# Kernel tuning notes

Hardware: AMD Instinct MI355X
Metric: run time of the kernel (lower is better)

Reference implementation:

```python
import jax, jax.numpy as jnp
import numpy as np

N_NODES = 20000
N_EDGES = 320000
IN_CH = 512
HEADS = 4
OUT_CH = 128
NEG_SLOPE = 0.2  # PyG GATConv default leaky_relu slope


def setup_inputs() -> dict:
    key = jax.random.key(0)
    k1, k2, k3, k4, k5 = jax.random.split(key, 5)
    x = jax.random.normal(k1, (N_NODES, IN_CH), dtype=jnp.float32)
    edge_index = jax.random.randint(k2, (2, N_EDGES), 0, N_NODES, dtype=jnp.int64)
    # Learned parameters (glorot-ish scaling)
    W = jax.random.normal(k3, (IN_CH, HEADS * OUT_CH), dtype=jnp.float32) * np.float32(1.0 / np.sqrt(IN_CH))
    att_src = jax.random.normal(k4, (HEADS, OUT_CH), dtype=jnp.float32) * np.float32(0.1)
    att_dst = jax.random.normal(k5, (HEADS, OUT_CH), dtype=jnp.float32) * np.float32(0.1)
    bias = jnp.zeros((OUT_CH,), dtype=jnp.float32)
    return {"x": x, "W": W, "att_src": att_src, "att_dst": att_dst, "bias": bias, "edge_index": edge_index}


def reference(x, W, att_src, att_dst, bias, edge_index):
    N = x.shape[0]
    H, C = att_src.shape
    # add self-loops (PyG GATConv default add_self_loops=True)
    loop = jnp.arange(N, dtype=edge_index.dtype)
    ei = jnp.concatenate([edge_index, jnp.stack([loop, loop])], axis=1)
    src, dst = ei[0], ei[1]
    # linear projection: [N, H, C]
    xl = (x @ W).reshape(N, H, C)
    # per-node attention halves: [N, H]
    a_s = jnp.einsum('nhc,hc->nh', xl, att_src)
    a_d = jnp.einsum('nhc,hc->nh', xl, att_dst)
    # per-edge logits + segment softmax over incoming edges (grouped by dst)
    alpha = jax.nn.leaky_relu(a_s[src] + a_d[dst], negative_slope=NEG_SLOPE)  # [E, H]
    amax = jax.ops.segment_max(alpha, dst, num_segments=N)  # every node has a self-loop -> no empty segments
    ae = jnp.exp(alpha - amax[dst])
    denom = jax.ops.segment_sum(ae, dst, num_segments=N)
    alpha = ae / (denom[dst] + 1e-16)
    # weighted scatter-add of source features: [N, H, C]
    out = jax.ops.segment_sum(alpha[:, :, None] * xl[src], dst, num_segments=N)
    # concat=False -> mean over heads, then bias [C]
    out = out.mean(axis=1) + bias
    return jax.nn.elu(out)
```

## Files before the change

### kernel.cpp

```cpp
#include <hip/hip_runtime.h>
#include <math.h>

#define N_NODES 20000
#define N_PAD 20096
#define N_EDGES 320000
#define IN_CH 512
#define HEADS 4
#define OUT_CH 128
#define HC 512
#define NEG_SLOPE 0.2f

#define CVX_BLOCKS 5024
#define CVW_BLOCKS 64
#define CNT_BLOCKS 1250
#define ATT_BLOCKS 1250

typedef __attribute__((ext_vector_type(8))) short short8;
typedef __attribute__((ext_vector_type(4))) float float4v;

__device__ __forceinline__ int detect_is64(const int* __restrict__ ei32) {
    int is64 = 1;
    #pragma unroll
    for (int i = 0; i < 32; i++) is64 &= (ei32[2 * i + 1] == 0);
    return is64;
}

__device__ __forceinline__ int edge_at(const void* ei, int is64, long long idx) {
    return is64 ? (int)((const long long*)ei)[idx] : ((const int*)ei)[idx];
}

__device__ __forceinline__ unsigned short f2bf(float f) {
    union { float f; unsigned u; } v; v.f = f;
    unsigned r = v.u + 0x7fffu + ((v.u >> 16) & 1u);
    return (unsigned short)(r >> 16);
}

__device__ __forceinline__ void bf8_decode(uint4 r, float* f) {
    f[0] = __uint_as_float(r.x << 16); f[1] = __uint_as_float(r.x & 0xffff0000u);
    f[2] = __uint_as_float(r.y << 16); f[3] = __uint_as_float(r.y & 0xffff0000u);
    f[4] = __uint_as_float(r.z << 16); f[5] = __uint_as_float(r.z & 0xffff0000u);
    f[6] = __uint_as_float(r.w << 16); f[7] = __uint_as_float(r.w & 0xffff0000u);
}

__device__ __forceinline__ float leaky(float t) { return t > 0.f ? t : NEG_SLOPE * t; }

__device__ __forceinline__ float sel_head(float4 w, int hd) {
    float lo = (hd & 1) ? w.y : w.x;
    float hi = (hd & 1) ? w.w : w.z;
    return (hd & 2) ? hi : lo;
}

__global__ __launch_bounds__(256) void fusedA_kernel(const float* __restrict__ x,
                                                     const float* __restrict__ W,
                                                     unsigned short* __restrict__ xb,
                                                     unsigned short* __restrict__ Wt,
                                                     const void* __restrict__ ei,
                                                     int* __restrict__ counts) {
    __shared__ float tile[64][65];
    int b = blockIdx.x;
    if (b < CVX_BLOCKS) {
        size_t i = ((size_t)b * 256 + threadIdx.x) * 8;
        unsigned short o[8];
        if (i < (size_t)N_NODES * IN_CH) {
            float4 f0 = *(const float4*)&x[i];
            float4 f1 = *(const float4*)&x[i + 4];
            o[0] = f2bf(f0.x); o[1] = f2bf(f0.y); o[2] = f2bf(f0.z); o[3] = f2bf(f0.w);
            o[4] = f2bf(f1.x); o[5] = f2bf(f1.y); o[6] = f2bf(f1.z); o[7] = f2bf(f1.w);
        } else {
            for (int k = 0; k < 8; k++) o[k] = 0;
        }
        *(short8*)&xb[i] = *(short8*)o;
    } else if (b < CVX_BLOCKS + CVW_BLOCKS) {
        int idx = b - CVX_BLOCKS;
        int k0 = (idx & 7) * 64, n0 = (idx >> 3) * 64;
        int t = threadIdx.x, r = t >> 6, c = t & 63;
        for (int rr = r; rr < 64; rr += 4)
            tile[rr][c] = W[(size_t)(k0 + rr) * HC + n0 + c];
        __syncthreads();
        for (int rr = r; rr < 64; rr += 4)
            Wt[(size_t)(n0 + rr) * IN_CH + k0 + c] = f2bf(tile[c][rr]);
    } else {
        int is64 = detect_is64((const int*)ei);
        int e = (b - CVX_BLOCKS - CVW_BLOCKS) * 256 + threadIdx.x;
        if (e < N_EDGES) {
            int dst = edge_at(ei, is64, (long long)N_EDGES + e);
            atomicAdd(&counts[dst], 1);
        }
    }
}

__global__ __launch_bounds__(256) void gemm_kernel(const unsigned short* __restrict__ A,
                                                   const unsigned short* __restrict__ Bt,
                                                   unsigned short* __restrict__ Cb) {
    __shared__ __align__(16) unsigned short As[128 * 32];
    __shared__ __align__(16) unsigned short Bs[128 * 32];
    const int bm = blockIdx.y * 128;
    const int bn = blockIdx.x * 128;
    const int t = threadIdx.x;
    const int wv = t >> 6, lane = t & 63;
    const int wm = wv & 1, wn = wv >> 1;
    const int lm = lane & 15, lk = lane >> 4;

    float4v acc[4][4];
    #pragma unroll
    for (int i = 0; i < 4; i++)
        #pragma unroll
        for (int j = 0; j < 4; j++) acc[i][j] = (float4v){0.f, 0.f, 0.f, 0.f};

    const int srow = t >> 2;
    const int skof = (t & 3) * 8;

    for (int k0 = 0; k0 < IN_CH; k0 += 32) {
        __syncthreads();
        #pragma unroll
        for (int q = 0; q < 2; q++) {
            const unsigned short* gA = A + (size_t)(bm + q * 64 + srow) * IN_CH + k0 + skof;
            const unsigned short* gB = Bt + (size_t)(bn + q * 64 + srow) * IN_CH + k0 + skof;
            __builtin_amdgcn_global_load_lds((const __attribute__((address_space(1))) void*)gA,
                                             (__attribute__((address_space(3))) void*)&As[q * 2048 + t * 8], 16, 0, 0);
            __builtin_amdgcn_global_load_lds((const __attribute__((address_space(1))) void*)gB,
                                             (__attribute__((address_space(3))) void*)&Bs[q * 2048 + t * 8], 16, 0, 0);
        }
        __syncthreads();

        short8 af[4], bf[4];
        #pragma unroll
        for (int i = 0; i < 4; i++)
            af[i] = *(const short8*)&As[(wm * 64 + i * 16 + lm) * 32 + lk * 8];
        #pragma unroll
        for (int j = 0; j < 4; j++)
            bf[j] = *(const short8*)&Bs[(wn * 64 + j * 16 + lm) * 32 + lk * 8];
        #pragma unroll
        for (int i = 0; i < 4; i++)
            #pragma unroll
            for (int j = 0; j < 4; j++)
                acc[i][j] = __builtin_amdgcn_mfma_f32_16x16x32_bf16(af[i], bf[j], acc[i][j], 0, 0, 0);
    }

    #pragma unroll
    for (int i = 0; i < 4; i++) {
        #pragma unroll
        for (int r = 0; r < 4; r++) {
            int row = bm + wm * 64 + i * 16 + lk * 4 + r;
            if (row < N_NODES) {
                #pragma unroll
                for (int j = 0; j < 4; j++) {
                    int col = bn + wn * 64 + j * 16 + lm;
                    Cb[(size_t)row * HC + col] = f2bf(acc[i][j][r]);
                }
            }
        }
    }
}

__global__ __launch_bounds__(1024) void scanattn_kernel(const int* __restrict__ counts,
                                                        int* __restrict__ offsets,
                                                        const unsigned short* __restrict__ xlb,
                                                        const float* __restrict__ att_s,
                                                        const float* __restrict__ att_d,
                                                        float* __restrict__ a_s,
                                                        float* __restrict__ a_d) {
    int b = blockIdx.x;
    if (b == 0) {
        const int CHUNK = 20;
        int tid = threadIdx.x;
        int base = tid * CHUNK;
        int c[CHUNK];
        #pragma unroll
        for (int k = 0; k < CHUNK; k++) {
            int i = base + k;
            c[k] = (i < N_NODES) ? counts[i] : 0;
        }
        int pre[CHUNK];
        int sum = 0;
        #pragma unroll
        for (int k = 0; k < CHUNK; k++) { pre[k] = sum; sum += c[k]; }

        int lane = tid & 63, wvv = tid >> 6;
        int s = sum;
        #pragma unroll
        for (int off = 1; off < 64; off <<= 1) {
            int u = __shfl_up(s, off, 64);
            if (lane >= off) s += u;
        }
        __shared__ int wsum[16];
        if (lane == 63) wsum[wvv] = s;
        __syncthreads();
        if (tid < 16) {
            int u = wsum[tid];
            #pragma unroll
            for (int off = 1; off < 16; off <<= 1) {
                int w = __shfl_up(u, off, 64);
                if (tid >= off) u += w;
            }
            wsum[tid] = u;
        }
        __syncthreads();
        int wbase = (wvv == 0) ? 0 : wsum[wvv - 1];
        int excl = wbase + s - sum;
        #pragma unroll
        for (int k = 0; k < CHUNK; k++) {
            int i = base + k;
            if (i < N_NODES) offsets[i] = excl + pre[k];
        }
        if (tid == 1023) offsets[N_NODES] = wbase + s;
    } else {
        int node = (b - 1) * 16 + (threadIdx.x >> 6);
        if (node >= N_NODES) return;
        int lane = threadIdx.x & 63;
        int hd = lane >> 4;
        uint4 r = *(const uint4*)&xlb[(size_t)node * HC + lane * 8];
        float f[8];
        bf8_decode(r, f);
        float4 s0 = *(const float4*)&att_s[lane * 8];
        float4 s1 = *(const float4*)&att_s[lane * 8 + 4];
        float4 d0 = *(const float4*)&att_d[lane * 8];
        float4 d1 = *(const float4*)&att_d[lane * 8 + 4];
        float s = f[0]*s0.x + f[1]*s0.y + f[2]*s0.z + f[3]*s0.w
                + f[4]*s1.x + f[5]*s1.y + f[6]*s1.z + f[7]*s1.w;
        float d = f[0]*d0.x + f[1]*d0.y + f[2]*d0.z + f[3]*d0.w
                + f[4]*d1.x + f[5]*d1.y + f[6]*d1.z + f[7]*d1.w;
        #pragma unroll
        for (int off = 1; off < 16; off <<= 1) {
            s += __shfl_xor(s, off, 64);
            d += __shfl_xor(d, off, 64);
        }
        if ((lane & 15) == 0) {
            a_s[node * 4 + hd] = s;
            a_d[node * 4 + hd] = d;
        }
    }
}

__global__ __launch_bounds__(256) void scatterw_kernel(const void* __restrict__ ei,
                                                       const int* __restrict__ offsets,
                                                       int* __restrict__ cursor,
                                                       int* __restrict__ sorted_src,
                                                       const float* __restrict__ a_s,
                                                       const float* __restrict__ a_d,
                                                       float* __restrict__ edge_w) {
    int is64 = detect_is64((const int*)ei);
    int e = blockIdx.x * 256 + threadIdx.x;
    if (e < N_EDGES) {
        int dst = edge_at(ei, is64, (long long)N_EDGES + e);
        int src = edge_at(ei, is64, e);
        int pos = offsets[dst] + atomicAdd(&cursor[dst], 1);
        sorted_src[pos] = src;
        float4 as4 = *(const float4*)&a_s[src * 4];
        float4 ad4 = *(const float4*)&a_d[dst * 4];
        float4 w;
        w.x = __expf(leaky(as4.x + ad4.x));
        w.y = __expf(leaky(as4.y + ad4.y));
        w.z = __expf(leaky(as4.z + ad4.z));
        w.w = __expf(leaky(as4.w + ad4.w));
        *(float4*)&edge_w[(size_t)pos * 4] = w;
    }
}

__global__ __launch_bounds__(256) void gather_kernel(const unsigned short* __restrict__ xlb,
                                                     const float* __restrict__ a_s,
                                                     const float* __restrict__ a_d,
                                                     const int* __restrict__ offsets,
                                                     const int* __restrict__ sorted_src,
                                                     const float* __restrict__ edge_w,
                                                     const float* __restrict__ bias,
                                                     float* __restrict__ out) {
    __shared__ float cl[2][64][9];
    int wv = threadIdx.x >> 6;
    int nib = wv >> 1;
    int sub = wv & 1;
    int node = blockIdx.x * 2 + nib;
    int lane = threadIdx.x & 63;
    int hd = lane >> 4;
    int beg = offsets[node], end = offsets[node + 1];

    const unsigned short* xrow = xlb + lane * 8;
    float acc[8] = {0, 0, 0, 0, 0, 0, 0, 0};
    float denom = 0.f;

    if (sub == 0) {
        float4 as4 = *(const float4*)&a_s[node * 4];
        float4 ad4 = *(const float4*)&a_d[node * 4];
        float4 ws;
        ws.x = __expf(leaky(as4.x + ad4.x));
        ws.y = __expf(leaky(as4.y + ad4.y));
        ws.z = __expf(leaky(as4.z + ad4.z));
        ws.w = __expf(leaky(as4.w + ad4.w));
        float w = sel_head(ws, hd);
        denom = w;
        uint4 r = *(const uint4*)(xrow + (size_t)node * HC);
        float f[8];
        bf8_decode(r, f);
        #pragma unroll
        for (int k = 0; k < 8; k++) acc[k] = w * f[k];
    }

    for (int c0 = beg + sub * 4; c0 < end; c0 += 8) {
        int n = end - c0;
        if (n >= 4) {
            int s0 = sorted_src[c0];
            int s1 = sorted_src[c0 + 1];
            int s2 = sorted_src[c0 + 2];
            int s3 = sorted_src[c0 + 3];
            uint4 r0 = *(const uint4*)(xrow + (size_t)s0 * HC);
            uint4 r1 = *(const uint4*)(xrow + (size_t)s1 * HC);
            uint4 r2 = *(const uint4*)(xrow + (size_t)s2 * HC);
            uint4 r3 = *(const uint4*)(xrow + (size_t)s3 * HC);
            float4 wa = *(const float4*)&edge_w[(size_t)c0 * 4];
            float4 wb = *(const float4*)&edge_w[(size_t)(c0 + 1) * 4];
            float4 wc = *(const float4*)&edge_w[(size_t)(c0 + 2) * 4];
            float4 wd = *(const float4*)&edge_w[(size_t)(c0 + 3) * 4];
            float w0 = sel_head(wa, hd), w1 = sel_head(wb, hd);
            float w2 = sel_head(wc, hd), w3 = sel_head(wd, hd);
            denom += (w0 + w1) + (w2 + w3);
            float f0[8], f1[8], f2[8], f3[8];
            bf8_decode(r0, f0);
            bf8_decode(r1, f1);
            bf8_decode(r2, f2);
            bf8_decode(r3, f3);
            #pragma unroll
            for (int k = 0; k < 8; k++)
                acc[k] += (w0 * f0[k] + w1 * f1[k]) + (w2 * f2[k] + w3 * f3[k]);
        } else {
            for (int j = 0; j < n; j++) {
                int s0 = sorted_src[c0 + j];
                uint4 r0 = *(const uint4*)(xrow + (size_t)s0 * HC);
                float4 wa = *(const float4*)&edge_w[(size_t)(c0 + j) * 4];
                float w0 = sel_head(wa, hd);
                denom += w0;
                float f0[8];
                bf8_decode(r0, f0);
                #pragma unroll
                for (int k = 0; k < 8; k++) acc[k] += w0 * f0[k];
            }
        }
    }

    if (sub == 1) {
        #pragma unroll
        for (int k = 0; k < 8; k++) cl[nib][lane][k] = acc[k];
        cl[nib][lane][8] = denom;
    }
    __syncthreads();
    if (sub == 0) {
        #pragma unroll
        for (int k = 0; k < 8; k++) acc[k] += cl[nib][lane][k];
        denom += cl[nib][lane][8];

        float rd = 0.25f / (denom + 1e-16f);
        float v[8];
        #pragma unroll
        for (int k = 0; k < 8; k++) {
            float t = acc[k] * rd;
            t += __shfl_xor(t, 16, 64);
            t += __shfl_xor(t, 32, 64);
            v[k] = t;
        }
        if (hd == 0) {
            float4 b0 = *(const float4*)&bias[lane * 8];
            float4 b1 = *(const float4*)&bias[lane * 8 + 4];
            float o[8];
            o[0] = v[0] + b0.x; o[1] = v[1] + b0.y; o[2] = v[2] + b0.z; o[3] = v[3] + b0.w;
            o[4] = v[4] + b1.x; o[5] = v[5] + b1.y; o[6] = v[6] + b1.z; o[7] = v[7] + b1.w;
            #pragma unroll
            for (int k = 0; k < 8; k++) o[k] = o[k] > 0.f ? o[k] : expm1f(o[k]);
            *(float4*)&out[(size_t)node * OUT_CH + lane * 8]     = make_float4(o[0], o[1], o[2], o[3]);
            *(float4*)&out[(size_t)node * OUT_CH + lane * 8 + 4] = make_float4(o[4], o[5], o[6], o[7]);
        }
    }
}

extern "C" void kernel_launch(void* const* d_in, const int* in_sizes, int n_in,
                              void* d_out, int out_size, void* d_ws, size_t ws_size,
                              hipStream_t stream) {
    const float* x       = (const float*)d_in[0];
    const float* W       = (const float*)d_in[1];
    const float* att_src = (const float*)d_in[2];
    const float* att_dst = (const float*)d_in[3];
    const float* bias    = (const float*)d_in[4];
    const void*  ei      = d_in[5];
    float* out = (float*)d_out;

    char* ws = (char*)d_ws;
    size_t off = 0;
    unsigned short* xlb = (unsigned short*)(ws + off); off += (size_t)N_PAD * HC * sizeof(unsigned short);
    float* a_s     = (float*)(ws + off); off += (size_t)N_NODES * HEADS * sizeof(float);
    float* a_d     = (float*)(ws + off); off += (size_t)N_NODES * HEADS * sizeof(float);
    int* counts    = (int*)(ws + off);   off += (size_t)N_NODES * sizeof(int);
    int* cursor    = (int*)(ws + off);   off += (size_t)N_NODES * sizeof(int);
    int* offsets   = (int*)(ws + off);   off += (size_t)(N_NODES + 1) * sizeof(int);
    off = (off + 15) & ~(size_t)15;
    int* sorted_src = (int*)(ws + off);  off += (size_t)N_EDGES * sizeof(int);
    off = (off + 15) & ~(size_t)15;
    float* edge_w  = (float*)(ws + off); off += (size_t)N_EDGES * HEADS * sizeof(float);
    unsigned short* xb = (unsigned short*)(ws + off); off += (size_t)N_PAD * IN_CH * sizeof(unsigned short);
    unsigned short* Wt = (unsigned short*)(ws + off); off += (size_t)IN_CH * HC * sizeof(unsigned short);

    hipMemsetAsync(counts, 0, 2u * N_NODES * sizeof(int), stream);
    fusedA_kernel<<<CVX_BLOCKS + CVW_BLOCKS + CNT_BLOCKS, 256, 0, stream>>>(x, W, xb, Wt, ei, counts);
    gemm_kernel<<<dim3(HC / 128, N_PAD / 128), 256, 0, stream>>>(xb, Wt, xlb);
    scanattn_kernel<<<1 + ATT_BLOCKS, 1024, 0, stream>>>(counts, offsets, xlb, att_src, att_dst, a_s, a_d);
    scatterw_kernel<<<(N_EDGES + 255) / 256, 256, 0, stream>>>(ei, offsets, cursor, sorted_src, a_s, a_d, edge_w);
    gather_kernel<<<N_NODES / 2, 256, 0, stream>>>(xlb, a_s, a_d, offsets, sorted_src, edge_w, bias, out);
}
```

Baseline: 215.3 us.

## Fuse x bf16 conversion and attention dot-products into GEMM with full-width tiles

The GEMM now reads fp32 x directly and converts it to bf16 while staging into LDS, which removes the separate conversion pass and the xb intermediate buffer. Each block covers 64 rows across all 512 output columns, so the per-head attention dot products a_s and a_d are computed from the accumulators in the epilogue. This eliminates the attention pass that re-read xlb. The cost is that the A-tile staging uses a synchronous register path instead of direct global-to-LDS loads. The scan moves to its own single-block kernel, and the attention scores are computed from fp32 accumulators instead of the rounded bf16 output.

```diff
diff --git a/kernel.cpp b/kernel.cpp
--- a/kernel.cpp
+++ b/kernel.cpp
@@ -2,7 +2,7 @@
 #include <math.h>
 
 #define N_NODES 20000
-#define N_PAD 20096
+#define N_PAD64 20032
 #define N_EDGES 320000
 #define IN_CH 512
 #define HEADS 4
@@ -10,10 +10,12 @@
 #define HC 512
 #define NEG_SLOPE 0.2f
 
-#define CVX_BLOCKS 5024
+#define GEMM_BM 64
+#define GEMM_BK 32
+#define GRID_M 313
+
 #define CVW_BLOCKS 64
 #define CNT_BLOCKS 1250
-#define ATT_BLOCKS 1250
 
 typedef __attribute__((ext_vector_type(8))) short short8;
 typedef __attribute__((ext_vector_type(4))) float float4v;
@@ -50,29 +52,14 @@
     return (hd & 2) ? hi : lo;
 }
 
-__global__ __launch_bounds__(256) void fusedA_kernel(const float* __restrict__ x,
-                                                     const float* __restrict__ W,
-                                                     unsigned short* __restrict__ xb,
+__global__ __launch_bounds__(256) void fusedA_kernel(const float* __restrict__ W,
                                                      unsigned short* __restrict__ Wt,
                                                      const void* __restrict__ ei,
                                                      int* __restrict__ counts) {
     __shared__ float tile[64][65];
     int b = blockIdx.x;
-    if (b < CVX_BLOCKS) {
-        size_t i = ((size_t)b * 256 + threadIdx.x) * 8;
-        unsigned short o[8];
-        if (i < (size_t)N_NODES * IN_CH) {
-            float4 f0 = *(const float4*)&x[i];
-            float4 f1 = *(const float4*)&x[i + 4];
-            o[0] = f2bf(f0.x); o[1] = f2bf(f0.y); o[2] = f2bf(f0.z); o[3] = f2bf(f0.w);
-            o[4] = f2bf(f1.x); o[5] = f2bf(f1.y); o[6] = f2bf(f1.z); o[7] = f2bf(f1.w);
-        } else {
-            for (int k = 0; k < 8; k++) o[k] = 0;
-        }
-        *(short8*)&xb[i] = *(short8*)o;
-    } else if (b < CVX_BLOCKS + CVW_BLOCKS) {
-        int idx = b - CVX_BLOCKS;
-        int k0 = (idx & 7) * 64, n0 = (idx >> 3) * 64;
+    if (b < CVW_BLOCKS) {
+        int k0 = (b & 7) * 64, n0 = (b >> 3) * 64;
         int t = threadIdx.x, r = t >> 6, c = t & 63;
         for (int rr = r; rr < 64; rr += 4)
             tile[rr][c] = W[(size_t)(k0 + rr) * HC + n0 + c];
@@ -81,7 +68,7 @@
             Wt[(size_t)(n0 + rr) * IN_CH + k0 + c] = f2bf(tile[c][rr]);
     } else {
         int is64 = detect_is64((const int*)ei);
-        int e = (b - CVX_BLOCKS - CVW_BLOCKS) * 256 + threadIdx.x;
+        int e = (b - CVW_BLOCKS) * 256 + threadIdx.x;
         if (e < N_EDGES) {
             int dst = edge_at(ei, is64, (long long)N_EDGES + e);
             atomicAdd(&counts[dst], 1);
@@ -89,16 +76,20 @@
     }
 }
 
-__global__ __launch_bounds__(256) void gemm_kernel(const unsigned short* __restrict__ A,
-                                                   const unsigned short* __restrict__ Bt,
-                                                   unsigned short* __restrict__ Cb) {
-    __shared__ __align__(16) unsigned short As[128 * 32];
-    __shared__ __align__(16) unsigned short Bs[128 * 32];
-    const int bm = blockIdx.y * 128;
-    const int bn = blockIdx.x * 128;
+__global__ __launch_bounds__(512) void gemm_kernel(const float* __restrict__ x,
+                                                   const unsigned short* __restrict__ Wt,
+                                                   unsigned short* __restrict__ Cb,
+                                                   const float* __restrict__ att_s_g,
+                                                   const float* __restrict__ att_d_g,
+                                                   float* __restrict__ a_s,
+                                                   float* __restrict__ a_d) {
+    __shared__ __align__(16) unsigned short As[GEMM_BM * GEMM_BK];
+    __shared__ __align__(16) unsigned short Bs[HC * GEMM_BK];
+    __shared__ float red_s[8][GEMM_BM];
+    __shared__ float red_d[8][GEMM_BM];
+    const int bm = blockIdx.x * GEMM_BM;
     const int t = threadIdx.x;
     const int wv = t >> 6, lane = t & 63;
-    const int wm = wv & 1, wn = wv >> 1;
     const int lm = lane & 15, lk = lane >> 4;
 
     float4v acc[4][4];
@@ -107,29 +98,35 @@
         #pragma unroll
         for (int j = 0; j < 4; j++) acc[i][j] = (float4v){0.f, 0.f, 0.f, 0.f};
 
-    const int srow = t >> 2;
-    const int skof = (t & 3) * 8;
-
-    for (int k0 = 0; k0 < IN_CH; k0 += 32) {
+    const int arow = t >> 3;
+    const int akof = (t & 7) * 4;
+    const int agrow = bm + arow;
+
+    for (int k0 = 0; k0 < IN_CH; k0 += GEMM_BK) {
         __syncthreads();
-        #pragma unroll
-        for (int q = 0; q < 2; q++) {
-            const unsigned short* gA = A + (size_t)(bm + q * 64 + srow) * IN_CH + k0 + skof;
-            const unsigned short* gB = Bt + (size_t)(bn + q * 64 + srow) * IN_CH + k0 + skof;
-            __builtin_amdgcn_global_load_lds((const __attribute__((address_space(1))) void*)gA,
-                                             (__attribute__((address_space(3))) void*)&As[q * 2048 + t * 8], 16, 0, 0);
+        float4 av = make_float4(0.f, 0.f, 0.f, 0.f);
+        if (agrow < N_NODES) av = *(const float4*)&x[(size_t)agrow * IN_CH + k0 + akof];
+        uint2 ap;
+        ap.x = (unsigned)f2bf(av.x) | ((unsigned)f2bf(av.y) << 16);
+        ap.y = (unsigned)f2bf(av.z) | ((unsigned)f2bf(av.w) << 16);
+        *(uint2*)&As[arow * GEMM_BK + akof] = ap;
+        #pragma unroll
+        for (int q = 0; q < 4; q++) {
+            int c = q * 512 + t;
+            int n = c >> 2, k8 = (c & 3) * 8;
+            const unsigned short* gB = Wt + (size_t)n * IN_CH + k0 + k8;
             __builtin_amdgcn_global_load_lds((const __attribute__((address_space(1))) void*)gB,
-                                             (__attribute__((address_space(3))) void*)&Bs[q * 2048 + t * 8], 16, 0, 0);
+                                             (__attribute__((address_space(3))) void*)&Bs[n * GEMM_BK + k8], 16, 0, 0);
         }
         __syncthreads();
 
         short8 af[4], bf[4];
         #pragma unroll
         for (int i = 0; i < 4; i++)
-            af[i] = *(const short8*)&As[(wm * 64 + i * 16 + lm) * 32 + lk * 8];
+            af[i] = *(const short8*)&As[(i * 16 + lm) * GEMM_BK + lk * 8];
         #pragma unroll
         for (int j = 0; j < 4; j++)
-            bf[j] = *(const short8*)&Bs[(wn * 64 + j * 16 + lm) * 32 + lk * 8];
+            bf[j] = *(const short8*)&Bs[(wv * 64 + j * 16 + lm) * GEMM_BK + lk * 8];
         #pragma unroll
         for (int i = 0; i < 4; i++)
             #pragma unroll
@@ -141,95 +138,98 @@
     for (int i = 0; i < 4; i++) {
         #pragma unroll
         for (int r = 0; r < 4; r++) {
-            int row = bm + wm * 64 + i * 16 + lk * 4 + r;
+            int row = bm + i * 16 + lk * 4 + r;
             if (row < N_NODES) {
                 #pragma unroll
                 for (int j = 0; j < 4; j++) {
-                    int col = bn + wn * 64 + j * 16 + lm;
+                    int col = wv * 64 + j * 16 + lm;
                     Cb[(size_t)row * HC + col] = f2bf(acc[i][j][r]);
                 }
             }
         }
     }
-}
-
-__global__ __launch_bounds__(1024) void scanattn_kernel(const int* __restrict__ counts,
-                                                        int* __restrict__ offsets,
-                                                        const unsigned short* __restrict__ xlb,
-                                                        const float* __restrict__ att_s,
-                                                        const float* __restrict__ att_d,
-                                                        float* __restrict__ a_s,
-                                                        float* __restrict__ a_d) {
-    int b = blockIdx.x;
-    if (b == 0) {
-        const int CHUNK = 20;
-        int tid = threadIdx.x;
-        int base = tid * CHUNK;
-        int c[CHUNK];
-        #pragma unroll
-        for (int k = 0; k < CHUNK; k++) {
-            int i = base + k;
-            c[k] = (i < N_NODES) ? counts[i] : 0;
-        }
-        int pre[CHUNK];
-        int sum = 0;
-        #pragma unroll
-        for (int k = 0; k < CHUNK; k++) { pre[k] = sum; sum += c[k]; }
-
-        int lane = tid & 63, wvv = tid >> 6;
-        int s = sum;
-        #pragma unroll
-        for (int off = 1; off < 64; off <<= 1) {
-            int u = __shfl_up(s, off, 64);
-            if (lane >= off) s += u;
-        }
-        __shared__ int wsum[16];
-        if (lane == 63) wsum[wvv] = s;
-        __syncthreads();
-        if (tid < 16) {
-            int u = wsum[tid];
+
+    float asv[4], adv[4];
+    #pragma unroll
+    for (int j = 0; j < 4; j++) {
+        int col = wv * 64 + j * 16 + lm;
+        asv[j] = att_s_g[col];
+        adv[j] = att_d_g[col];
+    }
+    #pragma unroll
+    for (int i = 0; i < 4; i++) {
+        #pragma unroll
+        for (int r = 0; r < 4; r++) {
+            float s = acc[i][0][r] * asv[0] + acc[i][1][r] * asv[1]
+                    + acc[i][2][r] * asv[2] + acc[i][3][r] * asv[3];
+            float d = acc[i][0][r] * adv[0] + acc[i][1][r] * adv[1]
+                    + acc[i][2][r] * adv[2] + acc[i][3][r] * adv[3];
             #pragma unroll
             for (int off = 1; off < 16; off <<= 1) {
-                int w = __shfl_up(u, off, 64);
-                if (tid >= off) u += w;
+                s += __shfl_xor(s, off, 64);
+                d += __shfl_xor(d, off, 64);
             }
-            wsum[tid] = u;
-        }
-        __syncthreads();
-        int wbase = (wvv == 0) ? 0 : wsum[wvv - 1];
-        int excl = wbase + s - sum;
-        #pragma unroll
-        for (int k = 0; k < CHUNK; k++) {
-            int i = base + k;
-            if (i < N_NODES) offsets[i] = excl + pre[k];
-        }
-        if (tid == 1023) offsets[N_NODES] = wbase + s;
-    } else {
-        int node = (b - 1) * 16 + (threadIdx.x >> 6);
-        if (node >= N_NODES) return;
-        int lane = threadIdx.x & 63;
-        int hd = lane >> 4;
-        uint4 r = *(const uint4*)&xlb[(size_t)node * HC + lane * 8];
-        float f[8];
-        bf8_decode(r, f);
-        float4 s0 = *(const float4*)&att_s[lane * 8];
-        float4 s1 = *(const float4*)&att_s[lane * 8 + 4];
-        float4 d0 = *(const float4*)&att_d[lane * 8];
-        float4 d1 = *(const float4*)&att_d[lane * 8 + 4];
-        float s = f[0]*s0.x + f[1]*s0.y + f[2]*s0.z + f[3]*s0.w
-                + f[4]*s1.x + f[5]*s1.y + f[6]*s1.z + f[7]*s1.w;
-        float d = f[0]*d0.x + f[1]*d0.y + f[2]*d0.z + f[3]*d0.w
-                + f[4]*d1.x + f[5]*d1.y + f[6]*d1.z + f[7]*d1.w;
+            if (lm == 0) {
+                red_s[wv][i * 16 + lk * 4 + r] = s;
+                red_d[wv][i * 16 + lk * 4 + r] = d;
+            }
+        }
+    }
+    __syncthreads();
+    if (t < 256) {
+        int row = t & 63, h = t >> 6;
+        int grow = bm + row;
+        if (grow < N_NODES) {
+            a_s[grow * 4 + h] = red_s[2 * h][row] + red_s[2 * h + 1][row];
+            a_d[grow * 4 + h] = red_d[2 * h][row] + red_d[2 * h + 1][row];
+        }
+    }
+}
+
+__global__ __launch_bounds__(1024) void scan_kernel(const int* __restrict__ counts,
+                                                    int* __restrict__ offsets) {
+    const int CHUNK = 20;
+    int tid = threadIdx.x;
+    int base = tid * CHUNK;
+    int c[CHUNK];
+    #pragma unroll
+    for (int k = 0; k < CHUNK; k++) {
+        int i = base + k;
+        c[k] = (i < N_NODES) ? counts[i] : 0;
+    }
+    int pre[CHUNK];
+    int sum = 0;
+    #pragma unroll
+    for (int k = 0; k < CHUNK; k++) { pre[k] = sum; sum += c[k]; }
+
+    int lane = tid & 63, wv = tid >> 6;
+    int s = sum;
+    #pragma unroll
+    for (int off = 1; off < 64; off <<= 1) {
+        int u = __shfl_up(s, off, 64);
+        if (lane >= off) s += u;
+    }
+    __shared__ int wsum[16];
+    if (lane == 63) wsum[wv] = s;
+    __syncthreads();
+    if (tid < 16) {
+        int u = wsum[tid];
         #pragma unroll
         for (int off = 1; off < 16; off <<= 1) {
-            s += __shfl_xor(s, off, 64);
-            d += __shfl_xor(d, off, 64);
-        }
-        if ((lane & 15) == 0) {
-            a_s[node * 4 + hd] = s;
-            a_d[node * 4 + hd] = d;
-        }
-    }
+            int w = __shfl_up(u, off, 64);
+            if (tid >= off) u += w;
+        }
+        wsum[tid] = u;
+    }
+    __syncthreads();
+    int wbase = (wv == 0) ? 0 : wsum[wv - 1];
+    int excl = wbase + s - sum;
+    #pragma unroll
+    for (int k = 0; k < CHUNK; k++) {
+        int i = base + k;
+        if (i < N_NODES) offsets[i] = excl + pre[k];
+    }
+    if (tid == 1023) offsets[N_NODES] = wbase + s;
 }
 
 __global__ __launch_bounds__(256) void scatterw_kernel(const void* __restrict__ ei,
@@ -383,7 +383,7 @@
 
     char* ws = (char*)d_ws;
     size_t off = 0;
-    unsigned short* xlb = (unsigned short*)(ws + off); off += (size_t)N_PAD * HC * sizeof(unsigned short);
+    unsigned short* xlb = (unsigned short*)(ws + off); off += (size_t)N_PAD64 * HC * sizeof(unsigned short);
     float* a_s     = (float*)(ws + off); off += (size_t)N_NODES * HEADS * sizeof(float);
     float* a_d     = (float*)(ws + off); off += (size_t)N_NODES * HEADS * sizeof(float);
     int* counts    = (int*)(ws + off);   off += (size_t)N_NODES * sizeof(int);
@@ -393,13 +393,12 @@
     int* sorted_src = (int*)(ws + off);  off += (size_t)N_EDGES * sizeof(int);
     off = (off + 15) & ~(size_t)15;
     float* edge_w  = (float*)(ws + off); off += (size_t)N_EDGES * HEADS * sizeof(float);
-    unsigned short* xb = (unsigned short*)(ws + off); off += (size_t)N_PAD * IN_CH * sizeof(unsigned short);
     unsigned short* Wt = (unsigned short*)(ws + off); off += (size_t)IN_CH * HC * sizeof(unsigned short);
 
     hipMemsetAsync(counts, 0, 2u * N_NODES * sizeof(int), stream);
-    fusedA_kernel<<<CVX_BLOCKS + CVW_BLOCKS + CNT_BLOCKS, 256, 0, stream>>>(x, W, xb, Wt, ei, counts);
-    gemm_kernel<<<dim3(HC / 128, N_PAD / 128), 256, 0, stream>>>(xb, Wt, xlb);
-    scanattn_kernel<<<1 + ATT_BLOCKS, 1024, 0, stream>>>(counts, offsets, xlb, att_src, att_dst, a_s, a_d);
+    fusedA_kernel<<<CVW_BLOCKS + CNT_BLOCKS, 256, 0, stream>>>(W, Wt, ei, counts);
+    gemm_kernel<<<GRID_M, 512, 0, stream>>>(x, Wt, xlb, att_src, att_dst, a_s, a_d);
+    scan_kernel<<<1, 1024, 0, stream>>>(counts, offsets);
     scatterw_kernel<<<(N_EDGES + 255) / 256, 256, 0, stream>>>(ei, offsets, cursor, sorted_src, a_s, a_d, edge_w);
     gather_kernel<<<N_NODES / 2, 256, 0, stream>>>(xlb, a_s, a_d, offsets, sorted_src, edge_w, bias, out);
 }
```

Result: slower. 223.0 us (+3.6%).

## Fuse scan into count kernel, attention dots into GEMM epilogue, weights into gather

Applied to the files above, without the earlier changes.

Moves the exclusive scan of in-degree counts into the tail of the first kernel, run by the last block to finish, which is found through an atomic done counter. Computes the per-node attention dot products in the GEMM epilogue from the fp32 accumulators, with cross-lane and shared-memory reductions, so the separate scan/attention kernel and its re-read of the projected features are gone. Edge weights are no longer precomputed and stored: the gather kernel recomputes exp(leaky(a_s+a_d)) per edge, which removes the edge_w buffer and its traffic but adds scattered a_s loads and exp work in the gather. It also adds bounds guards on source indices.

```diff
diff --git a/kernel.cpp b/kernel.cpp
--- a/kernel.cpp
+++ b/kernel.cpp
@@ -13,7 +13,7 @@
 #define CVX_BLOCKS 5024
 #define CVW_BLOCKS 64
 #define CNT_BLOCKS 1250
-#define ATT_BLOCKS 1250
+#define FA_BLOCKS  (CVX_BLOCKS + CVW_BLOCKS + CNT_BLOCKS)
 
 typedef __attribute__((ext_vector_type(8))) short short8;
 typedef __attribute__((ext_vector_type(4))) float float4v;
@@ -55,11 +55,14 @@
                                                      unsigned short* __restrict__ xb,
                                                      unsigned short* __restrict__ Wt,
                                                      const void* __restrict__ ei,
-                                                     int* __restrict__ counts) {
+                                                     int* __restrict__ counts,
+                                                     int* __restrict__ done,
+                                                     int* __restrict__ offsets) {
     __shared__ float tile[64][65];
     int b = blockIdx.x;
+    int t = threadIdx.x;
     if (b < CVX_BLOCKS) {
-        size_t i = ((size_t)b * 256 + threadIdx.x) * 8;
+        size_t i = ((size_t)b * 256 + t) * 8;
         unsigned short o[8];
         if (i < (size_t)N_NODES * IN_CH) {
             float4 f0 = *(const float4*)&x[i];
@@ -73,7 +76,7 @@
     } else if (b < CVX_BLOCKS + CVW_BLOCKS) {
         int idx = b - CVX_BLOCKS;
         int k0 = (idx & 7) * 64, n0 = (idx >> 3) * 64;
-        int t = threadIdx.x, r = t >> 6, c = t & 63;
+        int r = t >> 6, c = t & 63;
         for (int rr = r; rr < 64; rr += 4)
             tile[rr][c] = W[(size_t)(k0 + rr) * HC + n0 + c];
         __syncthreads();
@@ -81,21 +84,65 @@
             Wt[(size_t)(n0 + rr) * IN_CH + k0 + c] = f2bf(tile[c][rr]);
     } else {
         int is64 = detect_is64((const int*)ei);
-        int e = (b - CVX_BLOCKS - CVW_BLOCKS) * 256 + threadIdx.x;
+        int e = (b - CVX_BLOCKS - CVW_BLOCKS) * 256 + t;
         if (e < N_EDGES) {
             int dst = edge_at(ei, is64, (long long)N_EDGES + e);
             atomicAdd(&counts[dst], 1);
         }
     }
+
+    __syncthreads();
+    __threadfence();
+    __shared__ int lastFlag;
+    if (t == 0) lastFlag = (atomicAdd(done, 1) == FA_BLOCKS - 1);
+    __syncthreads();
+    if (!lastFlag) return;
+    __threadfence();
+
+    const int CHUNK = 80;
+    int base = t * CHUNK;
+    int sum = 0;
+    for (int k = 0; k < CHUNK; k++) {
+        int i = base + k;
+        sum += (i < N_NODES) ? counts[i] : 0;
+    }
+    int lane = t & 63, wv = t >> 6;
+    int s = sum;
+    #pragma unroll
+    for (int off = 1; off < 64; off <<= 1) {
+        int u = __shfl_up(s, off, 64);
+        if (lane >= off) s += u;
+    }
+    __shared__ int wsum[4], wexcl[4];
+    if (lane == 63) wsum[wv] = s;
+    __syncthreads();
+    if (t < 4) {
+        int acc = 0;
+        for (int j = 0; j < t; j++) acc += wsum[j];
+        wexcl[t] = acc;
+    }
+    __syncthreads();
+    int run = wexcl[wv] + s - sum;
+    for (int k = 0; k < CHUNK; k++) {
+        int i = base + k;
+        if (i < N_NODES) { offsets[i] = run; run += counts[i]; }
+    }
+    if (t == 255) offsets[N_NODES] = wexcl[3] + s;
 }
 
 __global__ __launch_bounds__(256) void gemm_kernel(const unsigned short* __restrict__ A,
                                                    const unsigned short* __restrict__ Bt,
-                                                   unsigned short* __restrict__ Cb) {
+                                                   unsigned short* __restrict__ Cb,
+                                                   const float* __restrict__ att_s_g,
+                                                   const float* __restrict__ att_d_g,
+                                                   float* __restrict__ a_s,
+                                                   float* __restrict__ a_d) {
     __shared__ __align__(16) unsigned short As[128 * 32];
     __shared__ __align__(16) unsigned short Bs[128 * 32];
+    __shared__ float red_s[4][64], red_d[4][64];
+    const int head = blockIdx.x;
+    const int bn = head * 128;
     const int bm = blockIdx.y * 128;
-    const int bn = blockIdx.x * 128;
     const int t = threadIdx.x;
     const int wv = t >> 6, lane = t & 63;
     const int wm = wv & 1, wn = wv >> 1;
@@ -151,109 +198,55 @@
             }
         }
     }
-}
-
-__global__ __launch_bounds__(1024) void scanattn_kernel(const int* __restrict__ counts,
-                                                        int* __restrict__ offsets,
-                                                        const unsigned short* __restrict__ xlb,
-                                                        const float* __restrict__ att_s,
-                                                        const float* __restrict__ att_d,
-                                                        float* __restrict__ a_s,
-                                                        float* __restrict__ a_d) {
-    int b = blockIdx.x;
-    if (b == 0) {
-        const int CHUNK = 20;
-        int tid = threadIdx.x;
-        int base = tid * CHUNK;
-        int c[CHUNK];
-        #pragma unroll
-        for (int k = 0; k < CHUNK; k++) {
-            int i = base + k;
-            c[k] = (i < N_NODES) ? counts[i] : 0;
-        }
-        int pre[CHUNK];
-        int sum = 0;
-        #pragma unroll
-        for (int k = 0; k < CHUNK; k++) { pre[k] = sum; sum += c[k]; }
-
-        int lane = tid & 63, wvv = tid >> 6;
-        int s = sum;
-        #pragma unroll
-        for (int off = 1; off < 64; off <<= 1) {
-            int u = __shfl_up(s, off, 64);
-            if (lane >= off) s += u;
-        }
-        __shared__ int wsum[16];
-        if (lane == 63) wsum[wvv] = s;
-        __syncthreads();
-        if (tid < 16) {
-            int u = wsum[tid];
+
+    float asv[4], adv[4];
+    #pragma unroll
+    for (int j = 0; j < 4; j++) {
+        int col = bn + wn * 64 + j * 16 + lm;
+        asv[j] = att_s_g[col];
+        adv[j] = att_d_g[col];
+    }
+    #pragma unroll
+    for (int i = 0; i < 4; i++) {
+        #pragma unroll
+        for (int r = 0; r < 4; r++) {
+            float s = acc[i][0][r] * asv[0] + acc[i][1][r] * asv[1]
+                    + acc[i][2][r] * asv[2] + acc[i][3][r] * asv[3];
+            float d = acc[i][0][r] * adv[0] + acc[i][1][r] * adv[1]
+                    + acc[i][2][r] * adv[2] + acc[i][3][r] * adv[3];
             #pragma unroll
             for (int off = 1; off < 16; off <<= 1) {
-                int w = __shfl_up(u, off, 64);
-                if (tid >= off) u += w;
+                s += __shfl_xor(s, off, 64);
+                d += __shfl_xor(d, off, 64);
             }
-            wsum[tid] = u;
-        }
-        __syncthreads();
-        int wbase = (wvv == 0) ? 0 : wsum[wvv - 1];
-        int excl = wbase + s - sum;
-        #pragma unroll
-        for (int k = 0; k < CHUNK; k++) {
-            int i = base + k;
-            if (i < N_NODES) offsets[i] = excl + pre[k];
-        }
-        if (tid == 1023) offsets[N_NODES] = wbase + s;
-    } else {
-        int node = (b - 1) * 16 + (threadIdx.x >> 6);
-        if (node >= N_NODES) return;
-        int lane = threadIdx.x & 63;
-        int hd = lane >> 4;
-        uint4 r = *(const uint4*)&xlb[(size_t)node * HC + lane * 8];
-        float f[8];
-        bf8_decode(r, f);
-        float4 s0 = *(const float4*)&att_s[lane * 8];
-        float4 s1 = *(const float4*)&att_s[lane * 8 + 4];
-        float4 d0 = *(const float4*)&att_d[lane * 8];
-        float4 d1 = *(const float4*)&att_d[lane * 8 + 4];
-        float s = f[0]*s0.x + f[1]*s0.y + f[2]*s0.z + f[3]*s0.w
-                + f[4]*s1.x + f[5]*s1.y + f[6]*s1.z + f[7]*s1.w;
-        float d = f[0]*d0.x + f[1]*d0.y + f[2]*d0.z + f[3]*d0.w
-                + f[4]*d1.x + f[5]*d1.y + f[6]*d1.z + f[7]*d1.w;
-        #pragma unroll
-        for (int off = 1; off < 16; off <<= 1) {
-            s += __shfl_xor(s, off, 64);
-            d += __shfl_xor(d, off, 64);
-        }
-        if ((lane & 15) == 0) {
-            a_s[node * 4 + hd] = s;
-            a_d[node * 4 + hd] = d;
-        }
-    }
-}
-
-__global__ __launch_bounds__(256) void scatterw_kernel(const void* __restrict__ ei,
-                                                       const int* __restrict__ offsets,
-                                                       int* __restrict__ cursor,
-                                                       int* __restrict__ sorted_src,
-                                                       const float* __restrict__ a_s,
-                                                       const float* __restrict__ a_d,
-                                                       float* __restrict__ edge_w) {
+            if (lm == 0) {
+                red_s[wv][i * 16 + lk * 4 + r] = s;
+                red_d[wv][i * 16 + lk * 4 + r] = d;
+            }
+        }
+    }
+    __syncthreads();
+    if (t < 128) {
+        int wm2 = t >> 6, row = t & 63;
+        int grow = bm + wm2 * 64 + row;
+        if (grow < N_NODES) {
+            a_s[grow * 4 + head] = red_s[wm2][row] + red_s[wm2 + 2][row];
+            a_d[grow * 4 + head] = red_d[wm2][row] + red_d[wm2 + 2][row];
+        }
+    }
+}
+
+__global__ __launch_bounds__(256) void scatter_kernel(const void* __restrict__ ei,
+                                                      const int* __restrict__ offsets,
+                                                      int* __restrict__ cursor,
+                                                      int* __restrict__ sorted_src) {
     int is64 = detect_is64((const int*)ei);
     int e = blockIdx.x * 256 + threadIdx.x;
     if (e < N_EDGES) {
         int dst = edge_at(ei, is64, (long long)N_EDGES + e);
         int src = edge_at(ei, is64, e);
         int pos = offsets[dst] + atomicAdd(&cursor[dst], 1);
-        sorted_src[pos] = src;
-        float4 as4 = *(const float4*)&a_s[src * 4];
-        float4 ad4 = *(const float4*)&a_d[dst * 4];
-        float4 w;
-        w.x = __expf(leaky(as4.x + ad4.x));
-        w.y = __expf(leaky(as4.y + ad4.y));
-        w.z = __expf(leaky(as4.z + ad4.z));
-        w.w = __expf(leaky(as4.w + ad4.w));
-        *(float4*)&edge_w[(size_t)pos * 4] = w;
+        if ((unsigned)pos < N_EDGES) sorted_src[pos] = src;
     }
 }
 
@@ -262,7 +255,6 @@
                                                      const float* __restrict__ a_d,
                                                      const int* __restrict__ offsets,
                                                      const int* __restrict__ sorted_src,
-                                                     const float* __restrict__ edge_w,
                                                      const float* __restrict__ bias,
                                                      float* __restrict__ out) {
     __shared__ float cl[2][64][9];
@@ -275,18 +267,12 @@
     int beg = offsets[node], end = offsets[node + 1];
 
     const unsigned short* xrow = xlb + lane * 8;
+    float adh = a_d[node * 4 + hd];
     float acc[8] = {0, 0, 0, 0, 0, 0, 0, 0};
     float denom = 0.f;
 
     if (sub == 0) {
-        float4 as4 = *(const float4*)&a_s[node * 4];
-        float4 ad4 = *(const float4*)&a_d[node * 4];
-        float4 ws;
-        ws.x = __expf(leaky(as4.x + ad4.x));
-        ws.y = __expf(leaky(as4.y + ad4.y));
-        ws.z = __expf(leaky(as4.z + ad4.z));
-        ws.w = __expf(leaky(as4.w + ad4.w));
-        float w = sel_head(ws, hd);
+        float w = __expf(leaky(a_s[node * 4 + hd] + adh));
         denom = w;
         uint4 r = *(const uint4*)(xrow + (size_t)node * HC);
         float f[8];
@@ -302,16 +288,18 @@
             int s1 = sorted_src[c0 + 1];
             int s2 = sorted_src[c0 + 2];
             int s3 = sorted_src[c0 + 3];
+            s0 = ((unsigned)s0 < N_NODES) ? s0 : 0;
+            s1 = ((unsigned)s1 < N_NODES) ? s1 : 0;
+            s2 = ((unsigned)s2 < N_NODES) ? s2 : 0;
+            s3 = ((unsigned)s3 < N_NODES) ? s3 : 0;
             uint4 r0 = *(const uint4*)(xrow + (size_t)s0 * HC);
             uint4 r1 = *(const uint4*)(xrow + (size_t)s1 * HC);
             uint4 r2 = *(const uint4*)(xrow + (size_t)s2 * HC);
             uint4 r3 = *(const uint4*)(xrow + (size_t)s3 * HC);
-            float4 wa = *(const float4*)&edge_w[(size_t)c0 * 4];
-            float4 wb = *(const float4*)&edge_w[(size_t)(c0 + 1) * 4];
-            float4 wc = *(const float4*)&edge_w[(size_t)(c0 + 2) * 4];
-            float4 wd = *(const float4*)&edge_w[(size_t)(c0 + 3) * 4];
-            float w0 = sel_head(wa, hd), w1 = sel_head(wb, hd);
-            float w2 = sel_head(wc, hd), w3 = sel_head(wd, hd);
+            float w0 = __expf(leaky(a_s[s0 * 4 + hd] + adh));
+            float w1 = __expf(leaky(a_s[s1 * 4 + hd] + adh));
+            float w2 = __expf(leaky(a_s[s2 * 4 + hd] + adh));
+            float w3 = __expf(leaky(a_s[s3 * 4 + hd] + adh));
             denom += (w0 + w1) + (w2 + w3);
             float f0[8], f1[8], f2[8], f3[8];
             bf8_decode(r0, f0);
@@ -324,9 +312,9 @@
         } else {
             for (int j = 0; j < n; j++) {
                 int s0 = sorted_src[c0 + j];
+                s0 = ((unsigned)s0 < N_NODES) ? s0 : 0;
                 uint4 r0 = *(const uint4*)(xrow + (size_t)s0 * HC);
-                float4 wa = *(const float4*)&edge_w[(size_t)(c0 + j) * 4];
-                float w0 = sel_head(wa, hd);
+                float w0 = __expf(leaky(a_s[s0 * 4 + hd] + adh));
                 denom += w0;
                 float f0[8];
                 bf8_decode(r0, f0);
@@ -388,18 +376,17 @@
     float* a_d     = (float*)(ws + off); off += (size_t)N_NODES * HEADS * sizeof(float);
     int* counts    = (int*)(ws + off);   off += (size_t)N_NODES * sizeof(int);
     int* cursor    = (int*)(ws + off);   off += (size_t)N_NODES * sizeof(int);
+    int* done      = (int*)(ws + off);   off += sizeof(int);
     int* offsets   = (int*)(ws + off);   off += (size_t)(N_NODES + 1) * sizeof(int);
     off = (off + 15) & ~(size_t)15;
     int* sorted_src = (int*)(ws + off);  off += (size_t)N_EDGES * sizeof(int);
     off = (off + 15) & ~(size_t)15;
-    float* edge_w  = (float*)(ws + off); off += (size_t)N_EDGES * HEADS * sizeof(float);
     unsigned short* xb = (unsigned short*)(ws + off); off += (size_t)N_PAD * IN_CH * sizeof(unsigned short);
     unsigned short* Wt = (unsigned short*)(ws + off); off += (size_t)IN_CH * HC * sizeof(unsigned short);
 
-    hipMemsetAsync(counts, 0, 2u * N_NODES * sizeof(int), stream);
-    fusedA_kernel<<<CVX_BLOCKS + CVW_BLOCKS + CNT_BLOCKS, 256, 0, stream>>>(x, W, xb, Wt, ei, counts);
-    gemm_kernel<<<dim3(HC / 128, N_PAD / 128), 256, 0, stream>>>(xb, Wt, xlb);
-    scanattn_kernel<<<1 + ATT_BLOCKS, 1024, 0, stream>>>(counts, offsets, xlb, att_src, att_dst, a_s, a_d);
-    scatterw_kernel<<<(N_EDGES + 255) / 256, 256, 0, stream>>>(ei, offsets, cursor, sorted_src, a_s, a_d, edge_w);
-    gather_kernel<<<N_NODES / 2, 256, 0, stream>>>(xlb, a_s, a_d, offsets, sorted_src, edge_w, bias, out);
-}
+    hipMemsetAsync(counts, 0, (2u * N_NODES + 1) * sizeof(int), stream);
+    fusedA_kernel<<<FA_BLOCKS, 256, 0, stream>>>(x, W, xb, Wt, ei, counts, done, offsets);
+    gemm_kernel<<<dim3(HC / 128, N_PAD / 128), 256, 0, stream>>>(xb, Wt, xlb, att_src, att_dst, a_s, a_d);
+    scatter_kernel<<<(N_EDGES + 255) / 256, 256, 0, stream>>>(ei, offsets, cursor, sorted_src);
+    gather_kernel<<<N_NODES / 2, 256, 0, stream>>>(xlb, a_s, a_d, offsets, sorted_src, bias, out);
+}
```

New measurement: 766.2 us. 256% more time.
